# Kernel optimization log

Hardware: AMD Instinct MI355X
Metric: run time of the kernel (lower is better)

Reference implementation:

```python
import jax, jax.numpy as jnp
import numpy as np

B, I_LEN, Q_LEN, H = 256, 256, 64, 512
MID, G, FLAT_OUT = 512, 1, 1024


def setup_inputs() -> dict:
    key = jax.random.key(0)
    ks = jax.random.split(key, 20)
    s = lambda k, sh: jax.random.normal(k, sh, dtype=jnp.float32) * 0.02
    inp = {
        'i_batch': jax.random.normal(ks[0], (B, I_LEN, H), dtype=jnp.float32),
        'q_batch': jax.random.normal(ks[1], (B, Q_LEN, H), dtype=jnp.float32),
        'i_mask': jax.random.bernoulli(ks[2], 0.1, (B, 1, 1, I_LEN)),
        'q_mask': jax.random.bernoulli(ks[3], 0.1, (B, 1, 1, Q_LEN)),
        # l_flatten (applied to i_feat) params
        'lf_w1': s(ks[4], (H, MID)), 'lf_b1': jnp.zeros((MID,), jnp.float32),
        'lf_w2': s(ks[5], (MID, G)), 'lf_b2': jnp.zeros((G,), jnp.float32),
        'lf_wm': s(ks[6], (H * G, FLAT_OUT)), 'lf_bm': jnp.zeros((FLAT_OUT,), jnp.float32),
        # i_flatten (applied to l_feat) params
        'if_w1': s(ks[7], (H, MID)), 'if_b1': jnp.zeros((MID,), jnp.float32),
        'if_w2': s(ks[8], (MID, G)), 'if_b2': jnp.zeros((G,), jnp.float32),
        'if_wm': s(ks[9], (H * G, FLAT_OUT)), 'if_bm': jnp.zeros((FLAT_OUT,), jnp.float32),
        # fh_h: Linear(1024, 512)
        'fh_w': s(ks[10], (FLAT_OUT, 512)), 'fh_b': jnp.zeros((512,), jnp.float32),
    }
    return inp


def _qkv_attention(query, key, value, mask):
    # query [B,Lq,H], key/value [B,Lk,H], mask [B,1,1,Lk] (True = pad)
    d_k = query.shape[-1]
    scores = jnp.einsum('bqh,bkh->bqk', query, key) / jnp.sqrt(jnp.asarray(d_k, query.dtype))
    scores = jnp.where(mask[:, 0], jnp.asarray(-65504.0, scores.dtype), scores)
    p_attn = jax.nn.softmax(scores, axis=-1)
    return jnp.einsum('bqk,bkh->bqh', p_attn, value)


def _att_flat(x, x_mask, w1, b1, w2, b2, wm, bm):
    # x [B,L,H], x_mask [B,1,1,L]
    att = jnp.maximum(x @ w1 + b1, 0.0) @ w2 + b2           # [B,L,G]
    att = jnp.where(x_mask[:, 0, 0, :, None], -1e9, att)
    att = jax.nn.softmax(att, axis=1)
    pooled = jnp.einsum('blg,blh->bgh', att, x).reshape(x.shape[0], -1)  # [B,G*H]
    return pooled @ wm + bm, att[..., 0]                    # att.squeeze() with G=1


def reference(i_batch, q_batch, i_mask, q_mask,
              lf_w1, lf_b1, lf_w2, lf_b2, lf_wm, lf_bm,
              if_w1, if_b1, if_w2, if_b2, if_wm, if_bm,
              fh_w, fh_b):
    i_feat = _qkv_attention(i_batch, q_batch, q_batch, q_mask)   # [B,I_LEN,H]
    i_feat, i_weight = _att_flat(i_feat, i_mask, lf_w1, lf_b1, lf_w2, lf_b2, lf_wm, lf_bm)
    l_feat = _qkv_attention(q_batch, i_batch, i_batch, i_mask)   # [B,Q_LEN,H]
    l_feat, _ = _att_flat(l_feat, q_mask, if_w1, if_b1, if_w2, if_b2, if_wm, if_bm)
    out = (l_feat + i_feat) @ fh_w + fh_b                        # [B,512]
    return out, i_weight
```

## Files before the change

kernel.cpp:

```cpp
#include <hip/hip_runtime.h>
#include <math.h>


#define SCALE 0.04419417382415922f

typedef __attribute__((ext_vector_type(8))) short short8;
typedef __attribute__((ext_vector_type(4))) float floatx4;

__device__ __forceinline__ unsigned short f2bf(float x) {
  unsigned u = __float_as_uint(x);
  unsigned r = u + 0x7FFFu + ((u >> 16) & 1u);
  return (unsigned short)(r >> 16);
}
__device__ __forceinline__ float bf2f(unsigned short h) {
  return __uint_as_float(((unsigned)h) << 16);
}
__device__ __forceinline__ unsigned pk2(float a, float b) {
  return (unsigned)f2bf(a) | ((unsigned)f2bf(b) << 16);
}

__device__ __forceinline__ float wave_max(float v) {
#pragma unroll
  for (int o = 32; o > 0; o >>= 1) v = fmaxf(v, __shfl_xor(v, o, 64));
  return v;
}
__device__ __forceinline__ float wave_sum(float v) {
#pragma unroll
  for (int o = 32; o > 0; o >>= 1) v += __shfl_xor(v, o, 64);
  return v;
}

#define GLD_LDS16(gptr, lptr)                                             \
  __builtin_amdgcn_global_load_lds(                                       \
      (const __attribute__((address_space(1))) void*)(gptr),              \
      (__attribute__((address_space(3))) void*)(lptr), 16, 0, 0)

__global__ __launch_bounds__(256) void k_prep(
    const float* __restrict__ qb, const float* __restrict__ lf_w1,
    const float* __restrict__ if_w1, const float* __restrict__ lf_wm,
    const float* __restrict__ if_wm, const float* __restrict__ fh_w,
    unsigned short* __restrict__ qb_bf, unsigned short* __restrict__ w1t_lf,
    unsigned short* __restrict__ w1t_if, unsigned short* __restrict__ wcat_t,
    unsigned short* __restrict__ fh_wt) {
  __shared__ __align__(16) char smem[64 * 65 * 4];
  const int idx = blockIdx.x, t = threadIdx.x;

  if (idx < 512) {
    float(*T)[65] = (float(*)[65])smem;
    const float* src;
    unsigned short* dst;
    int N, ds, koff, k0, n0;
    if (idx < 64) {
      src = lf_w1; dst = w1t_lf; N = 512; ds = 512; koff = 0;
      k0 = (idx & 7) * 64; n0 = (idx >> 3) * 64;
    } else if (idx < 128) {
      int l = idx - 64;
      src = if_w1; dst = w1t_if; N = 512; ds = 512; koff = 0;
      k0 = (l & 7) * 64; n0 = (l >> 3) * 64;
    } else if (idx < 256) {
      int l = idx - 128;
      src = lf_wm; dst = wcat_t; N = 1024; ds = 1024; koff = 0;
      k0 = (l & 7) * 64; n0 = (l >> 3) * 64;
    } else if (idx < 384) {
      int l = idx - 256;
      src = if_wm; dst = wcat_t; N = 1024; ds = 1024; koff = 512;
      k0 = (l & 7) * 64; n0 = (l >> 3) * 64;
    } else {
      int l = idx - 384;
      src = fh_w; dst = fh_wt; N = 512; ds = 1024; koff = 0;
      k0 = (l & 15) * 64; n0 = (l >> 4) * 64;
    }
#pragma unroll
    for (int i = 0; i < 16; i++) {
      int e = t + i * 256, r = e >> 6, c = e & 63;
      T[r][c] = src[(size_t)(k0 + r) * N + n0 + c];
    }
    __syncthreads();
#pragma unroll
    for (int i = 0; i < 8; i++) {
      int e = t + i * 256, r = e >> 5, c2 = (e & 31) * 2;
      *(unsigned*)&dst[(size_t)(n0 + r) * ds + koff + k0 + c2] =
          pk2(T[c2][r], T[c2 + 1][r]);
    }
  } else {
    int j = idx - 512;
    const float4* src = (const float4*)(qb + (size_t)j * 4096);
    uint2* dst = (uint2*)(qb_bf + (size_t)j * 4096);
#pragma unroll
    for (int i = 0; i < 4; i++) {
      int e = t + i * 256;
      float4 v = src[e];
      uint2 p;
      p.x = pk2(v.x, v.y);
      p.y = pk2(v.z, v.w);
      dst[e] = p;
    }
  }
}

__global__ __launch_bounds__(256) void k_scores_f(
    const float* __restrict__ ib, const unsigned short* __restrict__ qbf,
    const int* __restrict__ imask, const int* __restrict__ qmask,
    unsigned short* __restrict__ P1, unsigned short* __restrict__ P2,
    float* __restrict__ psum) {
  __shared__ unsigned short As[64 * 64];
  __shared__ unsigned short Bs[128 * 64];
  __shared__ __align__(16) unsigned short X[128 * 72];
  const int b = blockIdx.y, ic = blockIdx.x, i0 = ic * 128;
  const int t = threadIdx.x, w = t >> 6, lane = t & 63, c = lane & 15, qq = lane >> 4;

  floatx4 acc[4][2];
#pragma unroll
  for (int ti = 0; ti < 4; ti++)
#pragma unroll
    for (int tj = 0; tj < 2; tj++) acc[ti][tj] = (floatx4){0.f, 0.f, 0.f, 0.f};

  for (int k0 = 0; k0 < 512; k0 += 64) {
#pragma unroll
    for (int i = 0; i < 2; i++) {
      int s = i * 256 + t, row = s >> 3, src = (s & 7) ^ (row & 7);
      GLD_LDS16(qbf + ((size_t)b * 64 + row) * 512 + k0 + src * 8,
                &As[(i * 256 + w * 64) * 8]);
    }
#pragma unroll
    for (int i = 0; i < 8; i++) {
      int s = i * 256 + t, row = s >> 4, c4 = s & 15;
      float4 v = *(const float4*)&ib[((size_t)b * 256 + i0 + row) * 512 + k0 + c4 * 4];
      int gs = (c4 >> 1) ^ (row & 7), sub = c4 & 1;
      uint2 p;
      p.x = pk2(v.x, v.y);
      p.y = pk2(v.z, v.w);
      *(uint2*)&Bs[row * 64 + gs * 8 + sub * 4] = p;
    }
    __syncthreads();
#pragma unroll
    for (int kk = 0; kk < 2; kk++) {
      short8 a[4], bb[2];
#pragma unroll
      for (int ti = 0; ti < 4; ti++)
        a[ti] = *(const short8*)&As[(ti * 16 + c) * 64 + ((kk * 4 + qq) ^ (c & 7)) * 8];
#pragma unroll
      for (int tj = 0; tj < 2; tj++)
        bb[tj] = *(const short8*)&Bs[(w * 32 + tj * 16 + c) * 64 + ((kk * 4 + qq) ^ (c & 7)) * 8];
#pragma unroll
      for (int ti = 0; ti < 4; ti++)
#pragma unroll
        for (int tj = 0; tj < 2; tj++)
          acc[ti][tj] = __builtin_amdgcn_mfma_f32_16x16x32_bf16(a[ti], bb[tj], acc[ti][tj], 0, 0, 0);
    }
    __syncthreads();
  }

  const int il0 = w * 32 + c;
  int imsk0 = imask[b * 256 + i0 + il0];
  int imsk1 = imask[b * 256 + i0 + il0 + 16];
  int qm[4][4];
#pragma unroll
  for (int ti = 0; ti < 4; ti++)
#pragma unroll
    for (int rr = 0; rr < 4; rr++) qm[ti][rr] = qmask[b * 64 + ti * 16 + qq * 4 + rr];

#pragma unroll
  for (int ti = 0; ti < 4; ti++)
#pragma unroll
    for (int rr = 0; rr < 4; rr++) {
      int qv = ti * 16 + qq * 4 + rr;
      float e0 = imsk0 ? 0.f : __expf(acc[ti][0][rr] * SCALE);
      float e1 = imsk1 ? 0.f : __expf(acc[ti][1][rr] * SCALE);
      X[qv * 136 + il0] = f2bf(e0);
      X[qv * 136 + il0 + 16] = f2bf(e1);
      float s = e0 + e1;
#pragma unroll
      for (int o = 1; o <= 8; o <<= 1) s += __shfl_xor(s, o, 64);
      if (c == 0) psum[((size_t)(b * 64 + qv)) * 8 + ic * 4 + w] = s;
    }
  __syncthreads();
#pragma unroll
  for (int i = 0; i < 4; i++) {
    int e2 = t + i * 256, qv = e2 >> 4, g = e2 & 15;
    *(uint4*)&P2[((size_t)b * 64 + qv) * 256 + i0 + g * 8] = *(const uint4*)&X[qv * 136 + g * 8];
  }
  __syncthreads();

#pragma unroll
  for (int tj = 0; tj < 2; tj++) {
    float ev[4][4];
    float s1 = 0.f;
#pragma unroll
    for (int ti = 0; ti < 4; ti++)
#pragma unroll
      for (int rr = 0; rr < 4; rr++) {
        ev[ti][rr] = qm[ti][rr] ? 0.f : __expf(acc[ti][tj][rr] * SCALE);
        s1 += ev[ti][rr];
      }
    s1 += __shfl_xor(s1, 16, 64);
    s1 += __shfl_xor(s1, 32, 64);
    float inv = 1.f / s1;
    int il = il0 + tj * 16;
#pragma unroll
    for (int ti = 0; ti < 4; ti++)
#pragma unroll
      for (int rr = 0; rr < 4; rr++)
        X[il * 72 + ti * 16 + qq * 4 + rr] = f2bf(ev[ti][rr] * inv);
  }
  __syncthreads();
#pragma unroll
  for (int i = 0; i < 4; i++) {
    int e2 = t + i * 256, il = e2 >> 3, g = e2 & 7;
    *(uint4*)&P1[((size_t)b * 256 + i0 + il) * 64 + g * 8] = *(const uint4*)&X[il * 72 + g * 8];
  }
}

__global__ __launch_bounds__(256) void k_av2(const unsigned short* __restrict__ P2,
                                             const float* __restrict__ ib,
                                             const float* __restrict__ psum,
                                             unsigned short* __restrict__ lfeat) {
  __shared__ unsigned short As[64 * 64];
  __shared__ unsigned short Bs[128 * 64];
  __shared__ __align__(16) unsigned short Tb[64 * 128];
  const int b = blockIdx.y, n0 = blockIdx.x * 128;
  const int t = threadIdx.x, w = t >> 6, lane = t & 63, c = lane & 15, q = lane >> 4;
  const int wm = w >> 1, wn = w & 1;
  floatx4 acc[2][4];
#pragma unroll
  for (int ti = 0; ti < 2; ti++)
#pragma unroll
    for (int tj = 0; tj < 4; tj++) acc[ti][tj] = (floatx4){0.f, 0.f, 0.f, 0.f};

  for (int kc = 0; kc < 256; kc += 64) {
#pragma unroll
    for (int i = 0; i < 2; i++) {
      int s = i * 256 + t, row = s >> 3, src = (s & 7) ^ (row & 7);
      GLD_LDS16(P2 + ((size_t)b * 64 + row) * 256 + kc + src * 8, &As[(i * 256 + w * 64) * 8]);
    }
#pragma unroll
    for (int i = 0; i < 8; i++) {
      int e = i * 256 + t, tok = e >> 5, h4 = (e & 31) * 4;
      float4 v = *(const float4*)&ib[((size_t)b * 256 + kc + tok) * 512 + n0 + h4];
      uint2 p;
      p.x = pk2(v.x, v.y);
      p.y = pk2(v.z, v.w);
      int col = ((((h4 >> 3) ^ (tok >> 3)) & 15) << 3) | (h4 & 7);
      *(uint2*)&Tb[tok * 128 + col] = p;
    }
    __syncthreads();
#pragma unroll
    for (int i = 0; i < 4; i++) {
      int e = i * 256 + t, h = e >> 3, tc = (e & 7) * 8;
      int hg = h >> 3, ho = h & 7;
      unsigned y[8];
#pragma unroll
      for (int k = 0; k < 8; k++) {
        int r = tc + k;
        y[k] = Tb[r * 128 + (((hg ^ (r >> 3)) & 15) << 3) + ho];
      }
      uint4 vv;
      vv.x = y[0] | (y[1] << 16);
      vv.y = y[2] | (y[3] << 16);
      vv.z = y[4] | (y[5] << 16);
      vv.w = y[6] | (y[7] << 16);
      *(uint4*)&Bs[h * 64 + (((tc >> 3) ^ (h & 7)) << 3)] = vv;
    }
    __syncthreads();
#pragma unroll
    for (int kk = 0; kk < 2; kk++) {
      short8 a[2], bb[4];
#pragma unroll
      for (int ti = 0; ti < 2; ti++)
        a[ti] = *(const short8*)&As[(wm * 32 + ti * 16 + c) * 64 + ((kk * 4 + q) ^ (c & 7)) * 8];
#pragma unroll
      for (int tj = 0; tj < 4; tj++)
        bb[tj] = *(const short8*)&Bs[(wn * 64 + tj * 16 + c) * 64 + ((kk * 4 + q) ^ (c & 7)) * 8];
#pragma unroll
      for (int ti = 0; ti < 2; ti++)
#pragma unroll
        for (int tj = 0; tj < 4; tj++)
          acc[ti][tj] = __builtin_amdgcn_mfma_f32_16x16x32_bf16(a[ti], bb[tj], acc[ti][tj], 0, 0, 0);
    }
    __syncthreads();
  }
#pragma unroll
  for (int ti = 0; ti < 2; ti++)
#pragma unroll
    for (int rr = 0; rr < 4; rr++) {
      int m = wm * 32 + ti * 16 + q * 4 + rr;
      const float* ps = psum + ((size_t)(b * 64 + m)) * 8;
      float s = ps[0] + ps[1] + ps[2] + ps[3] + ps[4] + ps[5] + ps[6] + ps[7];
      float inv = 1.f / s;
      unsigned short* op = lfeat + ((size_t)b * 64 + m) * 512 + n0 + wn * 64;
#pragma unroll
      for (int tj = 0; tj < 4; tj++) op[tj * 16 + c] = f2bf(acc[ti][tj][rr] * inv);
    }
}

__global__ __launch_bounds__(256) void k_qbw1(const unsigned short* __restrict__ qbf,
                                              const unsigned short* __restrict__ W1t,
                                              unsigned short* __restrict__ qbW1T) {
  __shared__ unsigned short As[64 * 64];
  __shared__ unsigned short Bs[128 * 64];
  const int b = blockIdx.y, n0 = blockIdx.x * 128;
  const int t = threadIdx.x, w = t >> 6, lane = t & 63, c = lane & 15, q = lane >> 4;
  const int wm = w >> 1, wn = w & 1;
  floatx4 acc[2][4];
#pragma unroll
  for (int ti = 0; ti < 2; ti++)
#pragma unroll
    for (int tj = 0; tj < 4; tj++) acc[ti][tj] = (floatx4){0.f, 0.f, 0.f, 0.f};

  for (int k0 = 0; k0 < 512; k0 += 64) {
#pragma unroll
    for (int i = 0; i < 2; i++) {
      int s = i * 256 + t, row = s >> 3, src = (s & 7) ^ (row & 7);
      GLD_LDS16(qbf + ((size_t)b * 64 + row) * 512 + k0 + src * 8,
                &As[(i * 256 + w * 64) * 8]);
    }
#pragma unroll
    for (int i = 0; i < 4; i++) {
      int s = i * 256 + t, row = s >> 3, src = (s & 7) ^ (row & 7);
      GLD_LDS16(W1t + (size_t)(n0 + row) * 512 + k0 + src * 8,
                &Bs[(i * 256 + w * 64) * 8]);
    }
    __syncthreads();
#pragma unroll
    for (int kk = 0; kk < 2; kk++) {
      short8 a[2], bb[4];
#pragma unroll
      for (int ti = 0; ti < 2; ti++)
        a[ti] = *(const short8*)&As[(wm * 32 + ti * 16 + c) * 64 + ((kk * 4 + q) ^ (c & 7)) * 8];
#pragma unroll
      for (int tj = 0; tj < 4; tj++)
        bb[tj] = *(const short8*)&Bs[(wn * 64 + tj * 16 + c) * 64 + ((kk * 4 + q) ^ (c & 7)) * 8];
#pragma unroll
      for (int ti = 0; ti < 2; ti++)
#pragma unroll
        for (int tj = 0; tj < 4; tj++)
          acc[ti][tj] = __builtin_amdgcn_mfma_f32_16x16x32_bf16(a[ti], bb[tj], acc[ti][tj], 0, 0, 0);
    }
    __syncthreads();
  }
#pragma unroll
  for (int ti = 0; ti < 2; ti++)
#pragma unroll
    for (int tj = 0; tj < 4; tj++) {
      int n = n0 + wn * 64 + tj * 16 + c;
      int m = wm * 32 + ti * 16 + q * 4;
      uint2 p;
      p.x = pk2(acc[ti][tj][0], acc[ti][tj][1]);
      p.y = pk2(acc[ti][tj][2], acc[ti][tj][3]);
      *(uint2*)&qbW1T[((size_t)b * 512 + n) * 64 + m] = p;
    }
}

__global__ __launch_bounds__(256) void k_logits_i64(
    const unsigned short* __restrict__ P1, const unsigned short* __restrict__ qbW1T,
    const float* __restrict__ b1, const float* __restrict__ w2,
    float* __restrict__ outp) {
  __shared__ unsigned short As[128 * 64];
  __shared__ unsigned short Bs[128 * 64];
  __shared__ float red[2][128];
  const int b = blockIdx.y;
  const int mt = blockIdx.x & 1, nc = blockIdx.x >> 1;
  const int m0 = mt * 128, n0 = nc * 128;
  const int t = threadIdx.x, w = t >> 6, lane = t & 63, c = lane & 15, q = lane >> 4;
  const int wm = w >> 1, wn = w & 1;

#pragma unroll
  for (int i = 0; i < 4; i++) {
    int s = i * 256 + t, row = s >> 3, src = (s & 7) ^ (row & 7);
    GLD_LDS16(P1 + ((size_t)b * 256 + m0 + row) * 64 + src * 8, &As[(i * 256 + w * 64) * 8]);
  }
#pragma unroll
  for (int i = 0; i < 4; i++) {
    int s = i * 256 + t, row = s >> 3, src = (s & 7) ^ (row & 7);
    GLD_LDS16(qbW1T + ((size_t)b * 512 + n0 + row) * 64 + src * 8, &Bs[(i * 256 + w * 64) * 8]);
  }
  __syncthreads();
  floatx4 acc[4][4];
#pragma unroll
  for (int ti = 0; ti < 4; ti++)
#pragma unroll
    for (int tj = 0; tj < 4; tj++) acc[ti][tj] = (floatx4){0.f, 0.f, 0.f, 0.f};
#pragma unroll
  for (int kk = 0; kk < 2; kk++) {
    short8 a[4], bb[4];
#pragma unroll
    for (int ti = 0; ti < 4; ti++)
      a[ti] = *(const short8*)&As[(wm * 64 + ti * 16 + c) * 64 + ((kk * 4 + q) ^ (c & 7)) * 8];
#pragma unroll
    for (int tj = 0; tj < 4; tj++)
      bb[tj] = *(const short8*)&Bs[(wn * 64 + tj * 16 + c) * 64 + ((kk * 4 + q) ^ (c & 7)) * 8];
#pragma unroll
    for (int ti = 0; ti < 4; ti++)
#pragma unroll
      for (int tj = 0; tj < 4; tj++)
        acc[ti][tj] = __builtin_amdgcn_mfma_f32_16x16x32_bf16(a[ti], bb[tj], acc[ti][tj], 0, 0, 0);
  }

  float partial[4][4] = {};
#pragma unroll
  for (int tj = 0; tj < 4; tj++) {
    int n = n0 + wn * 64 + tj * 16 + c;
    float bia = b1[n], wwv = w2[n];
#pragma unroll
    for (int ti = 0; ti < 4; ti++)
#pragma unroll
      for (int r = 0; r < 4; r++)
        partial[ti][r] += fmaxf(acc[ti][tj][r] + bia, 0.f) * wwv;
  }
#pragma unroll
  for (int msk = 1; msk <= 8; msk <<= 1)
#pragma unroll
    for (int ti = 0; ti < 4; ti++)
#pragma unroll
      for (int r = 0; r < 4; r++)
        partial[ti][r] += __shfl_xor(partial[ti][r], msk, 64);
  if (c == 0) {
#pragma unroll
    for (int ti = 0; ti < 4; ti++)
#pragma unroll
      for (int r = 0; r < 4; r++)
        red[wn][wm * 64 + ti * 16 + q * 4 + r] = partial[ti][r];
  }
  __syncthreads();
  if (t < 128) outp[(size_t)nc * 65536 + b * 256 + m0 + t] = red[0][t] + red[1][t];
}

__global__ __launch_bounds__(256) void k_logits_part(
    const unsigned short* __restrict__ X, const unsigned short* __restrict__ W1t,
    const float* __restrict__ b1, const float* __restrict__ w2,
    float* __restrict__ outp, int M) {
  __shared__ unsigned short As[128 * 64];
  __shared__ unsigned short Bs[128 * 64];
  __shared__ float red[2][128];
  const int t = threadIdx.x, w = t >> 6, lane = t & 63;
  const int wm = w >> 1, wn = w & 1, c = lane & 15, q = lane >> 4;
  const int idx = blockIdx.x;
  const int m_tile = (idx & 7) + ((idx >> 5) << 3), nc = (idx >> 3) & 3;
  const int m0 = m_tile * 128, n0 = nc * 128;

  floatx4 acc[4][4];
#pragma unroll
  for (int ti = 0; ti < 4; ti++)
#pragma unroll
    for (int tj = 0; tj < 4; tj++) acc[ti][tj] = (floatx4){0.f, 0.f, 0.f, 0.f};

  for (int k0 = 0; k0 < 512; k0 += 64) {
#pragma unroll
    for (int it = 0; it < 4; it++) {
      int s = it * 256 + t, row = s >> 3, src = (s & 7) ^ (row & 7);
      GLD_LDS16(X + (size_t)(m0 + row) * 512 + k0 + src * 8, &As[(it * 256 + w * 64) * 8]);
      GLD_LDS16(W1t + (size_t)(n0 + row) * 512 + k0 + src * 8, &Bs[(it * 256 + w * 64) * 8]);
    }
    __syncthreads();
#pragma unroll
    for (int kk = 0; kk < 2; kk++) {
      short8 a[4], bb[4];
#pragma unroll
      for (int ti = 0; ti < 4; ti++)
        a[ti] = *(const short8*)&As[(wm * 64 + ti * 16 + c) * 64 + ((kk * 4 + q) ^ (c & 7)) * 8];
#pragma unroll
      for (int tj = 0; tj < 4; tj++)
        bb[tj] = *(const short8*)&Bs[(wn * 64 + tj * 16 + c) * 64 + ((kk * 4 + q) ^ (c & 7)) * 8];
#pragma unroll
      for (int ti = 0; ti < 4; ti++)
#pragma unroll
        for (int tj = 0; tj < 4; tj++)
          acc[ti][tj] = __builtin_amdgcn_mfma_f32_16x16x32_bf16(a[ti], bb[tj], acc[ti][tj], 0, 0, 0);
    }
    __syncthreads();
  }
  float partial[4][4] = {};
#pragma unroll
  for (int tj = 0; tj < 4; tj++) {
    int n = n0 + wn * 64 + tj * 16 + c;
    float bia = b1[n], wwv = w2[n];
#pragma unroll
    for (int ti = 0; ti < 4; ti++)
#pragma unroll
      for (int r = 0; r < 4; r++)
        partial[ti][r] += fmaxf(acc[ti][tj][r] + bia, 0.f) * wwv;
  }
#pragma unroll
  for (int msk = 1; msk <= 8; msk <<= 1)
#pragma unroll
    for (int ti = 0; ti < 4; ti++)
#pragma unroll
      for (int r = 0; r < 4; r++)
        partial[ti][r] += __shfl_xor(partial[ti][r], msk, 64);
  if (c == 0) {
#pragma unroll
    for (int ti = 0; ti < 4; ti++)
#pragma unroll
      for (int r = 0; r < 4; r++)
        red[wn][wm * 64 + ti * 16 + q * 4 + r] = partial[ti][r];
  }
  __syncthreads();
  if (t < 128) outp[(size_t)nc * M + m0 + t] = red[0][t] + red[1][t];
}

__global__ __launch_bounds__(256) void k_final_i(const float* __restrict__ lp,
                                                 const int* __restrict__ imask,
                                                 const unsigned short* __restrict__ P1,
                                                 const unsigned short* __restrict__ qbf,
                                                 float* __restrict__ iw_out,
                                                 unsigned short* __restrict__ pooled) {
  __shared__ float red4[4];
  __shared__ float ar[256];
  __shared__ float red[4][64];
  __shared__ float vsm[64];
  const int b = blockIdx.x, t = threadIdx.x;
  const int i = b * 256 + t;
  float x = lp[i] + lp[65536 + i] + lp[131072 + i] + lp[196608 + i];
  float v = imask[i] ? -1e9f : x;
  float wmx = wave_max(v);
  if ((t & 63) == 0) red4[t >> 6] = wmx;
  __syncthreads();
  float mx = fmaxf(fmaxf(red4[0], red4[1]), fmaxf(red4[2], red4[3]));
  __syncthreads();
  float e = __expf(v - mx);
  float ws = wave_sum(e);
  if ((t & 63) == 0) red4[t >> 6] = ws;
  __syncthreads();
  float s = red4[0] + red4[1] + red4[2] + red4[3];
  float p = e / s;
  iw_out[i] = p;
  ar[t] = p;
  __syncthreads();
  const int part = t >> 6, lane = t & 63;
  const unsigned short* Pb = P1 + ((size_t)b * 256 + part * 64) * 64 + lane;
  float s0 = 0.f, s1 = 0.f;
#pragma unroll 8
  for (int ii = 0; ii < 64; ii += 2) {
    s0 += ar[part * 64 + ii] * bf2f(Pb[(size_t)ii * 64]);
    s1 += ar[part * 64 + ii + 1] * bf2f(Pb[(size_t)(ii + 1) * 64]);
  }
  red[part][lane] = s0 + s1;
  __syncthreads();
  if (t < 64) vsm[t] = red[0][t] + red[1][t] + red[2][t] + red[3][t];
  __syncthreads();
  float a0 = 0.f, a1 = 0.f;
  const unsigned short* Xb = qbf + (size_t)b * 64 * 512 + 2 * t;
#pragma unroll 4
  for (int l = 0; l < 64; l++) {
    unsigned u = *(const unsigned*)&Xb[(size_t)l * 512];
    float a = vsm[l];
    a0 += a * bf2f((unsigned short)(u & 0xffff));
    a1 += a * bf2f((unsigned short)(u >> 16));
  }
  *(unsigned*)&pooled[(size_t)b * 1024 + 2 * t] = pk2(a0, a1);
}

__global__ __launch_bounds__(256) void k_final_l(const float* __restrict__ lp,
                                                 const int* __restrict__ qmask,
                                                 const unsigned short* __restrict__ lfeat,
                                                 unsigned short* __restrict__ pooled) {
  __shared__ float ar[64];
  const int b = blockIdx.x, t = threadIdx.x;
  if (t < 64) {
    const int i = b * 64 + t;
    float x = lp[i] + lp[16384 + i] + lp[32768 + i] + lp[49152 + i];
    float v = qmask[i] ? -1e9f : x;
    float mx = wave_max(v);
    float e = __expf(v - mx);
    float s = wave_sum(e);
    ar[t] = e / s;
  }
  __syncthreads();
  float a0 = 0.f, a1 = 0.f;
  const unsigned short* Xb = lfeat + (size_t)b * 64 * 512 + 2 * t;
#pragma unroll 4
  for (int l = 0; l < 64; l++) {
    unsigned u = *(const unsigned*)&Xb[(size_t)l * 512];
    float a = ar[l];
    a0 += a * bf2f((unsigned short)(u & 0xffff));
    a1 += a * bf2f((unsigned short)(u >> 16));
  }
  *(unsigned*)&pooled[(size_t)b * 1024 + 512 + 2 * t] = pk2(a0, a1);
}

__global__ __launch_bounds__(256) void k_egemm(const unsigned short* __restrict__ X,
                                               const unsigned short* __restrict__ Wt,
                                               const float* __restrict__ biasA,
                                               const float* __restrict__ biasB,
                                               float* __restrict__ outf,
                                               unsigned short* __restrict__ outbf,
                                               int N, int K) {
  __shared__ unsigned short As[64 * 64];
  __shared__ unsigned short Bs[64 * 64];
  const int n0 = blockIdx.x * 64, m0 = blockIdx.y * 64;
  const int t = threadIdx.x, w = t >> 6, lane = t & 63, c = lane & 15, q = lane >> 4;
  const int wm = w >> 1, wn = w & 1;
  floatx4 acc[2][2];
#pragma unroll
  for (int ti = 0; ti < 2; ti++)
#pragma unroll
    for (int tj = 0; tj < 2; tj++) acc[ti][tj] = (floatx4){0.f, 0.f, 0.f, 0.f};

  for (int k0 = 0; k0 < K; k0 += 64) {
#pragma unroll
    for (int i = 0; i < 2; i++) {
      int s = i * 256 + t, row = s >> 3, src = (s & 7) ^ (row & 7);
      GLD_LDS16(X + (size_t)(m0 + row) * K + k0 + src * 8, &As[(i * 256 + w * 64) * 8]);
      GLD_LDS16(Wt + (size_t)(n0 + row) * K + k0 + src * 8, &Bs[(i * 256 + w * 64) * 8]);
    }
    __syncthreads();
#pragma unroll
    for (int kk = 0; kk < 2; kk++) {
      short8 a[2], bb[2];
#pragma unroll
      for (int ti = 0; ti < 2; ti++)
        a[ti] = *(const short8*)&As[(wm * 32 + ti * 16 + c) * 64 + ((kk * 4 + q) ^ (c & 7)) * 8];
#pragma unroll
      for (int tj = 0; tj < 2; tj++)
        bb[tj] = *(const short8*)&Bs[(wn * 32 + tj * 16 + c) * 64 + ((kk * 4 + q) ^ (c & 7)) * 8];
#pragma unroll
      for (int ti = 0; ti < 2; ti++)
#pragma unroll
        for (int tj = 0; tj < 2; tj++)
          acc[ti][tj] = __builtin_amdgcn_mfma_f32_16x16x32_bf16(a[ti], bb[tj], acc[ti][tj], 0, 0, 0);
    }
    __syncthreads();
  }
#pragma unroll
  for (int tj = 0; tj < 2; tj++) {
    int n = n0 + wn * 32 + tj * 16 + c;
    float bias = biasA[n] + (biasB ? biasB[n] : 0.f);
#pragma unroll
    for (int ti = 0; ti < 2; ti++)
#pragma unroll
      for (int rr = 0; rr < 4; rr++) {
        int m = m0 + wm * 32 + ti * 16 + q * 4 + rr;
        float v = acc[ti][tj][rr] + bias;
        if (outbf) outbf[(size_t)m * N + n] = f2bf(v);
        else outf[(size_t)m * N + n] = v;
      }
  }
}

extern "C" void kernel_launch(void* const* d_in, const int* in_sizes, int n_in,
                              void* d_out, int out_size, void* d_ws, size_t ws_size,
                              hipStream_t stream) {
  const float* ib = (const float*)d_in[0];
  const float* qb = (const float*)d_in[1];
  const int* imask = (const int*)d_in[2];
  const int* qmask = (const int*)d_in[3];
  const float* lf_w1 = (const float*)d_in[4];
  const float* lf_b1 = (const float*)d_in[5];
  const float* lf_w2 = (const float*)d_in[6];
  const float* lf_wm = (const float*)d_in[8];
  const float* lf_bm = (const float*)d_in[9];
  const float* if_w1 = (const float*)d_in[10];
  const float* if_b1 = (const float*)d_in[11];
  const float* if_w2 = (const float*)d_in[12];
  const float* if_wm = (const float*)d_in[14];
  const float* if_bm = (const float*)d_in[15];
  const float* fh_w = (const float*)d_in[16];
  const float* fh_b = (const float*)d_in[17];
  float* out = (float*)d_out;

  float* lp_i = (float*)d_ws;
  float* lp_l = lp_i + 262144;
  float* att_i = lp_l + 65536;
  float* att_l = att_i + 65536;
  float* psum = att_l + 16384;
  unsigned short* P1 = (unsigned short*)(psum + 131072);
  unsigned short* P2 = P1 + 4194304;
  unsigned short* lfeat = P2 + 4194304;
  unsigned short* qb_bf = lfeat + 33554432;
  unsigned short* qbW1T = qb_bf + 8388608;
  unsigned short* ibT_unused = qbW1T + 8388608;
  unsigned short* w1t_lf = ibT_unused + 33554432;
  unsigned short* w1t_if = w1t_lf + 262144;
  unsigned short* wcat_t = w1t_if + 262144;
  unsigned short* fh_wt = wcat_t + 1048576;
  unsigned short* pooled_bf = fh_wt + 524288;
  unsigned short* F_bf = pooled_bf + 262144;

  k_prep<<<2560, 256, 0, stream>>>(qb, lf_w1, if_w1, lf_wm, if_wm, fh_w,
                                   qb_bf, w1t_lf, w1t_if, wcat_t, fh_wt);

  k_scores_f<<<dim3(2, 256), 256, 0, stream>>>(ib, qb_bf, imask, qmask, P1, P2, psum);
  k_av2<<<dim3(4, 256), 256, 0, stream>>>(P2, ib, psum, lfeat);
  k_qbw1<<<dim3(4, 256), 256, 0, stream>>>(qb_bf, w1t_lf, qbW1T);
  k_logits_i64<<<dim3(8, 256), 256, 0, stream>>>(P1, qbW1T, lf_b1, lf_w2, lp_i);
  k_logits_part<<<512, 256, 0, stream>>>(lfeat, w1t_if, if_b1, if_w2, lp_l, 16384);
  k_final_i<<<256, 256, 0, stream>>>(lp_i, imask, P1, qb_bf, out + 131072, pooled_bf);
  k_final_l<<<256, 256, 0, stream>>>(lp_l, qmask, lfeat, pooled_bf);

  k_egemm<<<dim3(16, 4), 256, 0, stream>>>(pooled_bf, wcat_t, lf_bm, if_bm,
                                           nullptr, F_bf, 1024, 1024);
  k_egemm<<<dim3(8, 4), 256, 0, stream>>>(F_bf, fh_wt, fh_b, nullptr,
                                          out, nullptr, 512, 1024);
}
```

Baseline: 381.3 us.

## Use hardware bf16 pack, alias LDS buffers, merge final kernels

Swaps the software round-to-nearest bf16 packing for the v_cvt_pk_bf16_f32 instruction. Aliases shared-memory buffers in k_scores_f and k_av2 to cut LDS footprint and allow more resident blocks, staging the transpose in registers so the B tile can be written back over Tb. Merges k_final_i and k_final_l into one launch with a block-index split, removing a kernel launch. The hardware conversion may round NaN or special values differently from the software version, and the aliasing depends on barrier placement being correct.

```diff
diff --git a/kernel.cpp b/kernel.cpp
--- a/kernel.cpp
+++ b/kernel.cpp
@@ -16,7 +16,9 @@
   return __uint_as_float(((unsigned)h) << 16);
 }
 __device__ __forceinline__ unsigned pk2(float a, float b) {
-  return (unsigned)f2bf(a) | ((unsigned)f2bf(b) << 16);
+  unsigned r;
+  asm("v_cvt_pk_bf16_f32 %0, %1, %2" : "=v"(r) : "v"(a), "v"(b));
+  return r;
 }
 
 __device__ __forceinline__ float wave_max(float v) {
@@ -103,9 +105,10 @@
     const int* __restrict__ imask, const int* __restrict__ qmask,
     unsigned short* __restrict__ P1, unsigned short* __restrict__ P2,
     float* __restrict__ psum) {
-  __shared__ unsigned short As[64 * 64];
-  __shared__ unsigned short Bs[128 * 64];
-  __shared__ __align__(16) unsigned short X[128 * 72];
+  __shared__ __align__(16) unsigned short U[64 * 64 + 128 * 64];
+  unsigned short* As = U;
+  unsigned short* Bs = U + 64 * 64;
+  unsigned short* X = U;
   const int b = blockIdx.y, ic = blockIdx.x, i0 = ic * 128;
   const int t = threadIdx.x, w = t >> 6, lane = t & 63, c = lane & 15, qq = lane >> 4;
 
@@ -216,8 +219,7 @@
                                              const float* __restrict__ psum,
                                              unsigned short* __restrict__ lfeat) {
   __shared__ unsigned short As[64 * 64];
-  __shared__ unsigned short Bs[128 * 64];
-  __shared__ __align__(16) unsigned short Tb[64 * 128];
+  __shared__ __align__(16) unsigned short Tb[128 * 64];
   const int b = blockIdx.y, n0 = blockIdx.x * 128;
   const int t = threadIdx.x, w = t >> 6, lane = t & 63, c = lane & 15, q = lane >> 4;
   const int wm = w >> 1, wn = w & 1;
@@ -244,6 +246,7 @@
       *(uint2*)&Tb[tok * 128 + col] = p;
     }
     __syncthreads();
+    uint4 vv[4];
 #pragma unroll
     for (int i = 0; i < 4; i++) {
       int e = i * 256 + t, h = e >> 3, tc = (e & 7) * 8;
@@ -254,14 +257,19 @@
         int r = tc + k;
         y[k] = Tb[r * 128 + (((hg ^ (r >> 3)) & 15) << 3) + ho];
       }
-      uint4 vv;
-      vv.x = y[0] | (y[1] << 16);
-      vv.y = y[2] | (y[3] << 16);
-      vv.z = y[4] | (y[5] << 16);
-      vv.w = y[6] | (y[7] << 16);
-      *(uint4*)&Bs[h * 64 + (((tc >> 3) ^ (h & 7)) << 3)] = vv;
-    }
-    __syncthreads();
+      vv[i].x = y[0] | (y[1] << 16);
+      vv[i].y = y[2] | (y[3] << 16);
+      vv[i].z = y[4] | (y[5] << 16);
+      vv[i].w = y[6] | (y[7] << 16);
+    }
+    __syncthreads();
+#pragma unroll
+    for (int i = 0; i < 4; i++) {
+      int e = i * 256 + t, h = e >> 3, tc = (e & 7) * 8;
+      *(uint4*)&Tb[h * 64 + (((tc >> 3) ^ (h & 7)) << 3)] = vv[i];
+    }
+    __syncthreads();
+    const unsigned short* Bs = Tb;
 #pragma unroll
     for (int kk = 0; kk < 2; kk++) {
       short8 a[2], bb[4];
@@ -498,84 +506,84 @@
   if (t < 128) outp[(size_t)nc * M + m0 + t] = red[0][t] + red[1][t];
 }
 
-__global__ __launch_bounds__(256) void k_final_i(const float* __restrict__ lp,
-                                                 const int* __restrict__ imask,
-                                                 const unsigned short* __restrict__ P1,
-                                                 const unsigned short* __restrict__ qbf,
-                                                 float* __restrict__ iw_out,
-                                                 unsigned short* __restrict__ pooled) {
+__global__ __launch_bounds__(256) void k_final(const float* __restrict__ lp_i,
+                                               const float* __restrict__ lp_l,
+                                               const int* __restrict__ imask,
+                                               const int* __restrict__ qmask,
+                                               const unsigned short* __restrict__ P1,
+                                               const unsigned short* __restrict__ qbf,
+                                               const unsigned short* __restrict__ lfeat,
+                                               float* __restrict__ iw_out,
+                                               unsigned short* __restrict__ pooled) {
   __shared__ float red4[4];
   __shared__ float ar[256];
   __shared__ float red[4][64];
   __shared__ float vsm[64];
-  const int b = blockIdx.x, t = threadIdx.x;
-  const int i = b * 256 + t;
-  float x = lp[i] + lp[65536 + i] + lp[131072 + i] + lp[196608 + i];
-  float v = imask[i] ? -1e9f : x;
-  float wmx = wave_max(v);
-  if ((t & 63) == 0) red4[t >> 6] = wmx;
-  __syncthreads();
-  float mx = fmaxf(fmaxf(red4[0], red4[1]), fmaxf(red4[2], red4[3]));
-  __syncthreads();
-  float e = __expf(v - mx);
-  float ws = wave_sum(e);
-  if ((t & 63) == 0) red4[t >> 6] = ws;
-  __syncthreads();
-  float s = red4[0] + red4[1] + red4[2] + red4[3];
-  float p = e / s;
-  iw_out[i] = p;
-  ar[t] = p;
-  __syncthreads();
-  const int part = t >> 6, lane = t & 63;
-  const unsigned short* Pb = P1 + ((size_t)b * 256 + part * 64) * 64 + lane;
-  float s0 = 0.f, s1 = 0.f;
+  const int t = threadIdx.x;
+  if (blockIdx.x < 256) {
+    const int b = blockIdx.x;
+    const int i = b * 256 + t;
+    float x = lp_i[i] + lp_i[65536 + i] + lp_i[131072 + i] + lp_i[196608 + i];
+    float v = imask[i] ? -1e9f : x;
+    float wmx = wave_max(v);
+    if ((t & 63) == 0) red4[t >> 6] = wmx;
+    __syncthreads();
+    float mx = fmaxf(fmaxf(red4[0], red4[1]), fmaxf(red4[2], red4[3]));
+    __syncthreads();
+    float e = __expf(v - mx);
+    float ws = wave_sum(e);
+    if ((t & 63) == 0) red4[t >> 6] = ws;
+    __syncthreads();
+    float s = red4[0] + red4[1] + red4[2] + red4[3];
+    float p = e / s;
+    iw_out[i] = p;
+    ar[t] = p;
+    __syncthreads();
+    const int part = t >> 6, lane = t & 63;
+    const unsigned short* Pb = P1 + ((size_t)b * 256 + part * 64) * 64 + lane;
+    float s0 = 0.f, s1 = 0.f;
 #pragma unroll 8
-  for (int ii = 0; ii < 64; ii += 2) {
-    s0 += ar[part * 64 + ii] * bf2f(Pb[(size_t)ii * 64]);
-    s1 += ar[part * 64 + ii + 1] * bf2f(Pb[(size_t)(ii + 1) * 64]);
-  }
-  red[part][lane] = s0 + s1;
-  __syncthreads();
-  if (t < 64) vsm[t] = red[0][t] + red[1][t] + red[2][t] + red[3][t];
-  __syncthreads();
-  float a0 = 0.f, a1 = 0.f;
-  const unsigned short* Xb = qbf + (size_t)b * 64 * 512 + 2 * t;
+    for (int ii = 0; ii < 64; ii += 2) {
+      s0 += ar[part * 64 + ii] * bf2f(Pb[(size_t)ii * 64]);
+      s1 += ar[part * 64 + ii + 1] * bf2f(Pb[(size_t)(ii + 1) * 64]);
+    }
+    red[part][lane] = s0 + s1;
+    __syncthreads();
+    if (t < 64) vsm[t] = red[0][t] + red[1][t] + red[2][t] + red[3][t];
+    __syncthreads();
+    float a0 = 0.f, a1 = 0.f;
+    const unsigned short* Xb = qbf + (size_t)b * 64 * 512 + 2 * t;
 #pragma unroll 4
-  for (int l = 0; l < 64; l++) {
-    unsigned u = *(const unsigned*)&Xb[(size_t)l * 512];
-    float a = vsm[l];
-    a0 += a * bf2f((unsigned short)(u & 0xffff));
-    a1 += a * bf2f((unsigned short)(u >> 16));
-  }
-  *(unsigned*)&pooled[(size_t)b * 1024 + 2 * t] = pk2(a0, a1);
-}
-
-__global__ __launch_bounds__(256) void k_final_l(const float* __restrict__ lp,
-                                                 const int* __restrict__ qmask,
-                                                 const unsigned short* __restrict__ lfeat,
-                                                 unsigned short* __restrict__ pooled) {
-  __shared__ float ar[64];
-  const int b = blockIdx.x, t = threadIdx.x;
-  if (t < 64) {
-    const int i = b * 64 + t;
-    float x = lp[i] + lp[16384 + i] + lp[32768 + i] + lp[49152 + i];
-    float v = qmask[i] ? -1e9f : x;
-    float mx = wave_max(v);
-    float e = __expf(v - mx);
-    float s = wave_sum(e);
-    ar[t] = e / s;
-  }
-  __syncthreads();
-  float a0 = 0.f, a1 = 0.f;
-  const unsigned short* Xb = lfeat + (size_t)b * 64 * 512 + 2 * t;
+    for (int l = 0; l < 64; l++) {
+      unsigned u = *(const unsigned*)&Xb[(size_t)l * 512];
+      float a = vsm[l];
+      a0 += a * bf2f((unsigned short)(u & 0xffff));
+      a1 += a * bf2f((unsigned short)(u >> 16));
+    }
+    *(unsigned*)&pooled[(size_t)b * 1024 + 2 * t] = pk2(a0, a1);
+  } else {
+    const int b = blockIdx.x - 256;
+    if (t < 64) {
+      const int i = b * 64 + t;
+      float x = lp_l[i] + lp_l[16384 + i] + lp_l[32768 + i] + lp_l[49152 + i];
+      float v = qmask[i] ? -1e9f : x;
+      float mx = wave_max(v);
+      float e = __expf(v - mx);
+      float s = wave_sum(e);
+      ar[t] = e / s;
+    }
+    __syncthreads();
+    float a0 = 0.f, a1 = 0.f;
+    const unsigned short* Xb = lfeat + (size_t)b * 64 * 512 + 2 * t;
 #pragma unroll 4
-  for (int l = 0; l < 64; l++) {
-    unsigned u = *(const unsigned*)&Xb[(size_t)l * 512];
-    float a = ar[l];
-    a0 += a * bf2f((unsigned short)(u & 0xffff));
-    a1 += a * bf2f((unsigned short)(u >> 16));
-  }
-  *(unsigned*)&pooled[(size_t)b * 1024 + 512 + 2 * t] = pk2(a0, a1);
+    for (int l = 0; l < 64; l++) {
+      unsigned u = *(const unsigned*)&Xb[(size_t)l * 512];
+      float a = ar[l];
+      a0 += a * bf2f((unsigned short)(u & 0xffff));
+      a1 += a * bf2f((unsigned short)(u >> 16));
+    }
+    *(unsigned*)&pooled[(size_t)b * 1024 + 512 + 2 * t] = pk2(a0, a1);
+  }
 }
 
 __global__ __launch_bounds__(256) void k_egemm(const unsigned short* __restrict__ X,
@@ -684,8 +692,8 @@
   k_qbw1<<<dim3(4, 256), 256, 0, stream>>>(qb_bf, w1t_lf, qbW1T);
   k_logits_i64<<<dim3(8, 256), 256, 0, stream>>>(P1, qbW1T, lf_b1, lf_w2, lp_i);
   k_logits_part<<<512, 256, 0, stream>>>(lfeat, w1t_if, if_b1, if_w2, lp_l, 16384);
-  k_final_i<<<256, 256, 0, stream>>>(lp_i, imask, P1, qb_bf, out + 131072, pooled_bf);
-  k_final_l<<<256, 256, 0, stream>>>(lp_l, qmask, lfeat, pooled_bf);
+  k_final<<<512, 256, 0, stream>>>(lp_i, lp_l, imask, qmask, P1, qb_bf, lfeat,
+                                   out + 131072, pooled_bf);
 
   k_egemm<<<dim3(16, 4), 256, 0, stream>>>(pooled_bf, wcat_t, lf_bm, if_bm,
                                            nullptr, F_bf, 1024, 1024);
```

Result: faster. 371.5 us (-2.6%).
